# Kernel tuning notes

Hardware: AMD Instinct MI355X
Metric: run time of the kernel (lower is better)

Reference implementation:

```python
import jax, jax.numpy as jnp
import numpy as np

K = 16  # neighbors

def _pdist2(a, b):
    # squared euclidean distances (B,N,M); same argsort order as torch.cdist
    return (jnp.sum(a * a, -1)[:, :, None] + jnp.sum(b * b, -1)[:, None, :]
            - 2.0 * jnp.einsum('bnd,bmd->bnm', a, b))

def _knn(xyz, k):
    d2 = jax.lax.stop_gradient(_pdist2(xyz, xyz))
    return jax.lax.top_k(-d2, k)[1]  # (B,N,k) smallest distances

_gather_f = jax.vmap(lambda f, i: f[:, i])  # feat (C,N), idx (...,) -> (C,...)
_gather_x = jax.vmap(lambda x, i: x[i])     # xyz (N,D), idx (...,) -> (...,D)

def _bn_act(x, g, b):
    # eval-mode BatchNorm (running_mean=0, running_var=1) folded to affine, + LeakyReLU(0.1)
    shp = (1, -1) + (1,) * (x.ndim - 2)
    return jax.nn.leaky_relu(x * g.reshape(shp) + b.reshape(shp), 0.1)

def _lfa(xyz, feat, idx, Wm, gm, bm, Ws, Wp, gp, bp):
    # xyz (B,N,3), feat (B,C,N), idx (B,N,K)
    neigh_feat = _gather_f(feat, idx)          # (B,C,N,K)
    neigh_xyz = _gather_x(xyz, idx)            # (B,N,K,3)
    center = xyz[:, :, None, :]
    diff = center - neigh_xyz
    dist = jnp.linalg.norm(diff, axis=-1, keepdims=True)
    rel = jnp.concatenate([diff, dist, jnp.broadcast_to(center, neigh_xyz.shape), neigh_xyz], axis=-1)
    rel = jnp.transpose(rel, (0, 3, 1, 2))     # (B,10,N,K)
    x = jnp.concatenate([neigh_feat, rel], axis=1)          # (B,C+10,N,K)
    x = _bn_act(jnp.einsum('oc,bcnk->bonk', Wm, x), gm, bm)  # (B,O,N,K)
    a = jax.nn.softmax(jnp.einsum('oc,bcnk->bonk', Ws, x), axis=3)
    x = jnp.sum(x * a, axis=3)                               # attentive pool over K -> (B,O,N)
    return _bn_act(jnp.einsum('oc,bcn->bon', Wp, x), gp, bp)

def _interp(src_xyz, src_feat, tgt_xyz):
    nn_idx = jnp.argmin(jax.lax.stop_gradient(_pdist2(tgt_xyz, src_xyz)), axis=-1)  # (B,N)
    return _gather_f(src_feat, nn_idx)  # (B,C,N)


def setup_inputs() -> dict:
    key = jax.random.key(0)
    ks = jax.random.split(key, 24)
    B, N, CIN, NC = 2, 8192, 6, 13
    M1, M2 = N // 2, N // 4
    w = lambda i, shp: jax.random.normal(ks[i], shp, jnp.float32) * 0.05
    ones = lambda c: jnp.ones((c,), jnp.float32)
    zeros = lambda c: jnp.zeros((c,), jnp.float32)
    inp = {
        'xyz': jax.random.uniform(ks[0], (B, N, 3), jnp.float32),
        'feat': jax.random.normal(ks[1], (B, N, CIN), jnp.float32),
        'sel1': jax.random.randint(ks[2], (B, M1), 0, N),
        'sel2': jax.random.randint(ks[3], (B, M2), 0, M1),
        'Wpre': w(4, (64, CIN)), 'gpre': ones(64), 'bpre': zeros(64),
        'W1m': w(5, (64, 74)), 'g1m': ones(64), 'b1m': zeros(64),
        'W1s': w(6, (64, 64)), 'W1p': w(7, (64, 64)), 'g1p': ones(64), 'b1p': zeros(64),
        'W2m': w(8, (128, 74)), 'g2m': ones(128), 'b2m': zeros(128),
        'W2s': w(9, (128, 128)), 'W2p': w(10, (128, 128)), 'g2p': ones(128), 'b2p': zeros(128),
        'W3m': w(11, (256, 138)), 'g3m': ones(256), 'b3m': zeros(256),
        'W3s': w(12, (256, 256)), 'W3p': w(13, (256, 256)), 'g3p': ones(256), 'b3p': zeros(256),
        'Wu2': w(14, (128, 384)), 'gu2': ones(128), 'bu2': zeros(128),
        'Wu1': w(15, (64, 192)), 'gu1': ones(64), 'bu1': zeros(64),
        'Wh1': w(16, (64, 64)), 'bh1': zeros(64),
        'Wh2': w(17, (NC, 64)), 'bh2': zeros(NC),
    }
    return inp


def reference(xyz, feat, sel1, sel2, Wpre, gpre, bpre,
              W1m, g1m, b1m, W1s, W1p, g1p, b1p,
              W2m, g2m, b2m, W2s, W2p, g2p, b2p,
              W3m, g3m, b3m, W3s, W3p, g3p, b3p,
              Wu2, gu2, bu2, Wu1, gu1, bu1,
              Wh1, bh1, Wh2, bh2):
    ft = jnp.transpose(feat, (0, 2, 1))                       # (B,Cin,N)
    x0 = _bn_act(jnp.einsum('oc,bcn->bon', Wpre, ft), gpre, bpre)
    n0 = _knn(xyz, K)
    x1 = _lfa(xyz, x0, n0, W1m, g1m, b1m, W1s, W1p, g1p, b1p)  # (B,64,N)
    xyz1 = _gather_x(xyz, sel1); f1 = _gather_f(x1, sel1)      # random downsample 0.5
    n1 = _knn(xyz1, K)
    x2 = _lfa(xyz1, f1, n1, W2m, g2m, b2m, W2s, W2p, g2p, b2p)  # (B,128,M1)
    xyz2 = _gather_x(xyz1, sel2); f2 = _gather_f(x2, sel2)
    n2 = _knn(xyz2, K)
    x3 = _lfa(xyz2, f2, n2, W3m, g3m, b3m, W3s, W3p, g3p, b3p)  # (B,256,M2)
    up2 = _interp(xyz2, x3, xyz1)
    d2 = _bn_act(jnp.einsum('oc,bcn->bon', Wu2, jnp.concatenate([up2, x2], 1)), gu2, bu2)
    up1 = _interp(xyz1, d2, xyz)
    d1 = _bn_act(jnp.einsum('oc,bcn->bon', Wu1, jnp.concatenate([up1, x1], 1)), gu1, bu1)
    h = jax.nn.leaky_relu(jnp.einsum('oc,bcn->bon', Wh1, d1) + bh1[None, :, None], 0.1)
    logits = jnp.einsum('oc,bcn->bon', Wh2, h) + bh2[None, :, None]
    return jnp.transpose(logits, (0, 2, 1))                    # (B,N,num_classes)
```

## Files before the change

kernel.cpp:

```cpp
#include <hip/hip_runtime.h>
#include <hip/hip_bf16.h>

#pragma clang fp contract(off)

typedef unsigned long long ull;

__device__ __forceinline__ float lrelu(float v) { return v >= 0.0f ? v : 0.1f * v; }

__device__ __forceinline__ float sumsq3(float x, float y, float z) {
    return ((x * x) + (y * y)) + (z * z);
}

__device__ __forceinline__ float dot3fma(float ax, float ay, float az,
                                         float bx, float by, float bz) {
    float d = ax * bx;
    d = __builtin_fmaf(ay, by, d);
    d = __builtin_fmaf(az, bz, d);
    return d;
}

__device__ __forceinline__ float distf(float qn, float sn, float dot) {
    float s = qn + sn;
    return __builtin_fmaf(-2.0f, dot, s);
}

__device__ __forceinline__ ull packkey(float d, int i) {
    unsigned u = __float_as_uint(d);
    u = (u & 0x80000000u) ? ~u : (u | 0x80000000u);
    return ((ull)u << 32) | (unsigned)i;
}

__device__ __forceinline__ ull shfl_xor_u64(ull v, int mask) {
    int lo = __shfl_xor((int)(v & 0xffffffffull), mask);
    int hi = __shfl_xor((int)(v >> 32), mask);
    return ((ull)(unsigned)hi << 32) | (unsigned)lo;
}

__device__ __forceinline__ void cswap64(ull& x, ull& y) {
    bool sw = y < x;
    ull lo = sw ? y : x;
    ull hi = sw ? x : y;
    x = lo; y = hi;
}

__device__ __forceinline__ ull min64(ull a, ull b) { return a < b ? a : b; }

__global__ void k_pre(const float* __restrict__ feat, const float* __restrict__ W,
                      const float* __restrict__ g, const float* __restrict__ bb,
                      float* __restrict__ x0) {
    int p = blockIdx.x * blockDim.x + threadIdx.x;
    if (p >= 2 * 8192) return;
    const float* f = feat + (size_t)p * 6;
    float fv[6];
#pragma unroll
    for (int c = 0; c < 6; ++c) fv[c] = f[c];
    float* out = x0 + (size_t)p * 64;
    for (int o = 0; o < 64; ++o) {
        float s = 0.0f;
#pragma unroll
        for (int c = 0; c < 6; ++c) s = __builtin_fmaf(W[o * 6 + c], fv[c], s);
        float v = s * g[o];
        v = v + bb[o];
        out[o] = lrelu(v);
    }
}

__global__ void k_wt(const float* __restrict__ W, float* __restrict__ WT, int M, int K) {
    int i = blockIdx.x * 256 + threadIdx.x;
    if (i >= M * K) return;
    int o = i / K, c = i - o * K;
    WT[c * M + o] = W[i];
}

template <int LPQ, int TS>
__launch_bounds__(256)
__global__ void k_knn_reg(const float* __restrict__ xyz, int* __restrict__ out_idx, int Npts) {
    constexpr int QPB = 256 / LPQ;
    __shared__ float4 sp[TS];
    int b = blockIdx.y;
    int tid = threadIdx.x;
    int qi = tid / LPQ;
    int l = tid % LPQ;
    int q = blockIdx.x * QPB + qi;
    const float* X = xyz + (size_t)b * Npts * 3;
    float qx = X[q * 3], qy = X[q * 3 + 1], qz = X[q * 3 + 2];
    float qn = sumsq3(qx, qy, qz);

    ull key[16];
#pragma unroll
    for (int u = 0; u < 16; ++u) key[u] = ~0ull;
    ull p0 = ~0ull, p1 = ~0ull, p2 = ~0ull, p3 = ~0ull;
    int cnt = 0;
    float tau_d = INFINITY;

    auto merge = [&]() {
        cswap64(p0, p2); cswap64(p1, p3); cswap64(p0, p1);
        cswap64(p2, p3); cswap64(p1, p2);
        key[12] = min64(key[12], p3);
        key[13] = min64(key[13], p2);
        key[14] = min64(key[14], p1);
        key[15] = min64(key[15], p0);
#pragma unroll
        for (int dstep = 8; dstep >= 1; dstep >>= 1) {
#pragma unroll
            for (int i = 0; i < 16; ++i) {
                if (!(i & dstep)) cswap64(key[i], key[i + dstep]);
            }
        }
        p0 = p1 = p2 = p3 = ~0ull;
        cnt = 0;
        ull t = key[15];
#pragma unroll
        for (int mask = 1; mask < LPQ; mask <<= 1) t = min64(t, shfl_xor_u64(t, mask));
        unsigned hu = (unsigned)(t >> 32);
        unsigned fb = (hu & 0x80000000u) ? (hu & 0x7fffffffu) : ~hu;
        tau_d = (hu == 0xffffffffu) ? INFINITY : __uint_as_float(fb);
    };

    for (int t0 = 0; t0 < Npts; t0 += TS) {
        __syncthreads();
        for (int j = tid; j < TS; j += 256) {
            int i = t0 + j;
            float px = X[i * 3], py = X[i * 3 + 1], pz = X[i * 3 + 2];
            sp[j] = make_float4(px, py, pz, sumsq3(px, py, pz));
        }
        __syncthreads();
        for (int j = l; j < TS; j += LPQ) {
            float4 p = sp[j];
            float d = distf(qn, p.w, dot3fma(qx, qy, qz, p.x, p.y, p.z));
            if (d <= tau_d) {
                p3 = p2; p2 = p1; p1 = p0;
                p0 = packkey(d, t0 + j);
                ++cnt;
            }
            if (__any(cnt >= 4)) merge();
        }
    }
    if (__any(cnt > 0)) merge();

    for (int mask = 1; mask < LPQ; mask <<= 1) {
        ull ok[16];
#pragma unroll
        for (int i = 0; i < 16; ++i) ok[i] = shfl_xor_u64(key[15 - i], mask);
#pragma unroll
        for (int i = 0; i < 16; ++i) key[i] = min64(ok[i], key[i]);
#pragma unroll
        for (int dstep = 8; dstep >= 1; dstep >>= 1) {
#pragma unroll
            for (int i = 0; i < 16; ++i) {
                if (!(i & dstep)) cswap64(key[i], key[i + dstep]);
            }
        }
    }

    if (l == 0) {
        int* o = out_idx + ((size_t)b * Npts + q) * 16;
#pragma unroll
        for (int u = 0; u < 16; ++u) o[u] = (int)(unsigned)(key[u] & 0xffffffffull);
    }
}

template <int C>
__global__ void k_gather(const float* __restrict__ src_xyz, const float* __restrict__ src_feat,
                         const int* __restrict__ sel, float* __restrict__ dst_xyz,
                         float* __restrict__ dst_feat, int M, int Nsrc) {
    int b = blockIdx.y, m = blockIdx.x;
    int s = sel[(size_t)b * M + m];
    const float* fx = src_xyz + ((size_t)b * Nsrc + s) * 3;
    const float* ff = src_feat + ((size_t)b * Nsrc + s) * C;
    float* dx = dst_xyz + ((size_t)b * M + m) * 3;
    float* df = dst_feat + ((size_t)b * M + m) * C;
    if (threadIdx.x < 3) dx[threadIdx.x] = fx[threadIdx.x];
    for (int c = threadIdx.x; c < C; c += blockDim.x) df[c] = ff[c];
}

template <int CIN, int COUT, int NCOL>
__launch_bounds__(256)
__global__ void k_lfa(const float* __restrict__ xyz, const float* __restrict__ feat,
                      const int* __restrict__ kn,
                      const float* __restrict__ WmT, const float* __restrict__ gm, const float* __restrict__ bm,
                      const float* __restrict__ WsT,
                      const float* __restrict__ WpT, const float* __restrict__ gp, const float* __restrict__ bp,
                      float* __restrict__ outf, int Npts) {
    constexpr int CR = CIN + 10;
    constexpr int PPB = NCOL / 16;
    constexpr int RT = COUT / 16;
    constexpr int CT = NCOL / 16;
    constexpr int TPG = 16 / CT;
    constexpr int BUFR = (CR > COUT) ? CR : COUT;
    __shared__ float buf[BUFR * NCOL];
    int b = blockIdx.y, tid = threadIdx.x;
    int n0 = blockIdx.x * PPB;
    const float* X = xyz + (size_t)b * Npts * 3;

    {
        constexpr int TPC = 256 / NCOL;
        int jl = tid % NCOL;
        int cp = tid / NCOL;
        int n = n0 + (jl >> 4);
        int k = jl & 15;
        int nbr = kn[((size_t)b * Npts + n) * 16 + k];
        const float* fr = feat + ((size_t)b * Npts + nbr) * CIN;
        for (int c = cp; c < CIN; c += TPC) buf[c * NCOL + jl] = fr[c];
        if (cp == 0) {
            float cx = X[n * 3], cy = X[n * 3 + 1], cz = X[n * 3 + 2];
            float nx = X[nbr * 3], ny = X[nbr * 3 + 1], nz = X[nbr * 3 + 2];
            float dx = cx - nx, dy = cy - ny, dz = cz - nz;
            float dn = sqrtf(sumsq3(dx, dy, dz));
            buf[(CIN + 0) * NCOL + jl] = dx; buf[(CIN + 1) * NCOL + jl] = dy;
            buf[(CIN + 2) * NCOL + jl] = dz; buf[(CIN + 3) * NCOL + jl] = dn;
            buf[(CIN + 4) * NCOL + jl] = cx; buf[(CIN + 5) * NCOL + jl] = cy;
            buf[(CIN + 6) * NCOL + jl] = cz; buf[(CIN + 7) * NCOL + jl] = nx;
            buf[(CIN + 8) * NCOL + jl] = ny; buf[(CIN + 9) * NCOL + jl] = nz;
        }
    }
    __syncthreads();

    int tx = tid & 15, ty = tid >> 4;
    float acc[RT][CT];
#pragma unroll
    for (int r = 0; r < RT; ++r)
#pragma unroll
        for (int cc = 0; cc < CT; ++cc) acc[r][cc] = 0.0f;

    for (int c = 0; c < CR; ++c) {
        float a[RT], bv[CT];
#pragma unroll
        for (int r4 = 0; r4 < RT; r4 += 4)
            *reinterpret_cast<float4*>(&a[r4]) =
                *reinterpret_cast<const float4*>(&WmT[c * COUT + ty * RT + r4]);
#pragma unroll
        for (int c4 = 0; c4 < CT; c4 += 4)
            *reinterpret_cast<float4*>(&bv[c4]) =
                *reinterpret_cast<const float4*>(&buf[c * NCOL + tx * CT + c4]);
#pragma unroll
        for (int r = 0; r < RT; ++r)
#pragma unroll
            for (int cc = 0; cc < CT; ++cc)
                acc[r][cc] = __builtin_fmaf(a[r], bv[cc], acc[r][cc]);
    }
    __syncthreads();
#pragma unroll
    for (int r = 0; r < RT; ++r) {
        int o = ty * RT + r;
        float gg = gm[o], bbv = bm[o];
#pragma unroll
        for (int cc = 0; cc < CT; ++cc) {
            float v = acc[r][cc] * gg;
            v = v + bbv;
            buf[o * NCOL + tx * CT + cc] = lrelu(v);
        }
    }
    __syncthreads();

#pragma unroll
    for (int r = 0; r < RT; ++r)
#pragma unroll
        for (int cc = 0; cc < CT; ++cc) acc[r][cc] = 0.0f;
    for (int c = 0; c < COUT; ++c) {
        float a[RT], bv[CT];
#pragma unroll
        for (int r4 = 0; r4 < RT; r4 += 4)
            *reinterpret_cast<float4*>(&a[r4]) =
                *reinterpret_cast<const float4*>(&WsT[c * COUT + ty * RT + r4]);
#pragma unroll
        for (int c4 = 0; c4 < CT; c4 += 4)
            *reinterpret_cast<float4*>(&bv[c4]) =
                *reinterpret_cast<const float4*>(&buf[c * NCOL + tx * CT + c4]);
#pragma unroll
        for (int r = 0; r < RT; ++r)
#pragma unroll
            for (int cc = 0; cc < CT; ++cc)
                acc[r][cc] = __builtin_fmaf(a[r], bv[cc], acc[r][cc]);
    }
    float pwv[RT];
#pragma unroll
    for (int r = 0; r < RT; ++r) {
        int o = ty * RT + r;
        float m = acc[r][0];
#pragma unroll
        for (int cc = 1; cc < CT; ++cc) m = fmaxf(m, acc[r][cc]);
#pragma unroll
        for (int mask = 1; mask < TPG; mask <<= 1) m = fmaxf(m, __shfl_xor(m, mask));
        float e[CT]; float ps = 0.0f;
#pragma unroll
        for (int cc = 0; cc < CT; ++cc) { e[cc] = expf(acc[r][cc] - m); ps = ps + e[cc]; }
        float tot = ps;
#pragma unroll
        for (int mask = 1; mask < TPG; mask <<= 1) tot = tot + __shfl_xor(tot, mask);
        float pw = 0.0f;
#pragma unroll
        for (int cc = 0; cc < CT; ++cc) {
            float a_ = e[cc] / tot;
            float t = buf[o * NCOL + tx * CT + cc] * a_;
            pw = pw + t;
        }
#pragma unroll
        for (int mask = 1; mask < TPG; mask <<= 1) pw = pw + __shfl_xor(pw, mask);
        pwv[r] = pw;
    }
    __syncthreads();
    if (tx % TPG == 0) {
        int pt = tx / TPG;
#pragma unroll
        for (int r = 0; r < RT; ++r) buf[(ty * RT + r) * PPB + pt] = pwv[r];
    }
    __syncthreads();

    constexpr int NOUT = (COUT * PPB) / 256;
    constexpr int PSTEP = 256 / COUT;
    int o = tid % COUT;
    int pbase = tid / COUT;
    float sacc[NOUT];
#pragma unroll
    for (int u = 0; u < NOUT; ++u) sacc[u] = 0.0f;
    for (int c = 0; c < COUT; ++c) {
        float wv = WpT[c * COUT + o];
#pragma unroll
        for (int u = 0; u < NOUT; ++u)
            sacc[u] = __builtin_fmaf(wv, buf[c * PPB + pbase + u * PSTEP], sacc[u]);
    }
    float gg = gp[o], bbv = bp[o];
#pragma unroll
    for (int u = 0; u < NOUT; ++u) {
        float v = sacc[u] * gg;
        v = v + bbv;
        int p = pbase + u * PSTEP;
        outf[((size_t)b * Npts + n0 + p) * COUT + o] = lrelu(v);
    }
}

template <int LPQ, int TS>
__launch_bounds__(256)
__global__ void k_nn_par(const float* __restrict__ tgt, const float* __restrict__ src,
                         int* __restrict__ nn, int Mt, int Ms) {
    constexpr int QPB = 256 / LPQ;
    __shared__ float4 sp[TS];
    int b = blockIdx.y;
    int tid = threadIdx.x;
    int qi = tid / LPQ;
    int l = tid % LPQ;
    int q = blockIdx.x * QPB + qi;
    const float* T = tgt + (size_t)b * Mt * 3;
    const float* S = src + (size_t)b * Ms * 3;
    float qx = T[q * 3], qy = T[q * 3 + 1], qz = T[q * 3 + 2];
    float qn = sumsq3(qx, qy, qz);
    float bd = INFINITY; int bi = 0x7fffffff;
    for (int t0 = 0; t0 < Ms; t0 += TS) {
        __syncthreads();
        for (int j = tid; j < TS; j += 256) {
            int i = t0 + j;
            float px = S[i * 3], py = S[i * 3 + 1], pz = S[i * 3 + 2];
            sp[j] = make_float4(px, py, pz, sumsq3(px, py, pz));
        }
        __syncthreads();
        for (int j = l; j < TS; j += LPQ) {
            float4 p = sp[j];
            float d = distf(qn, p.w, dot3fma(qx, qy, qz, p.x, p.y, p.z));
            if (d < bd) { bd = d; bi = t0 + j; }
        }
    }
#pragma unroll
    for (int s = LPQ / 2; s; s >>= 1) {
        float od = __shfl_xor(bd, s);
        int oi = __shfl_xor(bi, s);
        bool better = (od < bd) || ((od == bd) && (oi < bi));
        bd = better ? od : bd;
        bi = better ? oi : bi;
    }
    if (l == 0) nn[(size_t)b * Mt + q] = bi;
}

template <int CSRC, int CSKIP, int COUT>
__global__ void k_up(const float* __restrict__ srcf, const float* __restrict__ skipf,
                     const int* __restrict__ nn,
                     const float* __restrict__ W, const float* __restrict__ g, const float* __restrict__ bb,
                     float* __restrict__ outf, int Mt, int Ms) {
    __shared__ float fin[CSRC + CSKIP];
    int b = blockIdx.y, n = blockIdx.x, tid = threadIdx.x;
    int j = nn[(size_t)b * Mt + n];
    const float* fs = srcf + ((size_t)b * Ms + j) * CSRC;
    const float* fk = skipf + ((size_t)b * Mt + n) * CSKIP;
    for (int c = tid; c < CSRC; c += blockDim.x) fin[c] = fs[c];
    for (int c = tid; c < CSKIP; c += blockDim.x) fin[CSRC + c] = fk[c];
    __syncthreads();
    for (int o = tid; o < COUT; o += blockDim.x) {
        const float* wr = W + (size_t)o * (CSRC + CSKIP);
        float s = 0.0f;
        for (int c = 0; c < CSRC + CSKIP; ++c) s = __builtin_fmaf(wr[c], fin[c], s);
        float v = s * g[o]; v = v + bb[o];
        outf[((size_t)b * Mt + n) * COUT + o] = lrelu(v);
    }
}

__global__ void k_u1head(const float* __restrict__ srcf, const float* __restrict__ skipf,
                         const int* __restrict__ nn,
                         const float* __restrict__ Wu1, const float* __restrict__ gu1, const float* __restrict__ bu1,
                         const float* __restrict__ Wh1, const float* __restrict__ bh1,
                         const float* __restrict__ Wh2, const float* __restrict__ bh2,
                         float* __restrict__ out, int Mt, int Ms) {
    __shared__ float fin[192];
    __shared__ float d1[64];
    __shared__ float h[64];
    int b = blockIdx.y, n = blockIdx.x, tid = threadIdx.x;
    int j = nn[(size_t)b * Mt + n];
    const float* fs = srcf + ((size_t)b * Ms + j) * 128;
    const float* fk = skipf + ((size_t)b * Mt + n) * 64;
    for (int c = tid; c < 128; c += 64) fin[c] = fs[c];
    fin[128 + tid] = fk[tid];
    __syncthreads();
    {
        const float* wr = Wu1 + (size_t)tid * 192;
        float s = 0.0f;
        for (int c = 0; c < 192; ++c) s = __builtin_fmaf(wr[c], fin[c], s);
        float v = s * gu1[tid]; v = v + bu1[tid];
        d1[tid] = lrelu(v);
    }
    __syncthreads();
    {
        const float* wr = Wh1 + (size_t)tid * 64;
        float s = 0.0f;
        for (int c = 0; c < 64; ++c) s = __builtin_fmaf(wr[c], d1[c], s);
        float v = s + bh1[tid];
        h[tid] = lrelu(v);
    }
    __syncthreads();
    if (tid < 13) {
        const float* wr = Wh2 + (size_t)tid * 64;
        float s = 0.0f;
        for (int c = 0; c < 64; ++c) s = __builtin_fmaf(wr[c], h[c], s);
        out[((size_t)b * Mt + n) * 13 + tid] = s + bh2[tid];
    }
}

extern "C" void kernel_launch(void* const* d_in, const int* in_sizes, int n_in,
                              void* d_out, int out_size, void* d_ws, size_t ws_size,
                              hipStream_t stream) {
    const float* xyz  = (const float*)d_in[0];
    const float* feat = (const float*)d_in[1];
    const int*   sel1 = (const int*)d_in[2];
    const int*   sel2 = (const int*)d_in[3];
    const float* Wpre = (const float*)d_in[4];
    const float* gpre = (const float*)d_in[5];
    const float* bpre = (const float*)d_in[6];
    const float* W1m  = (const float*)d_in[7];
    const float* g1m  = (const float*)d_in[8];
    const float* b1m  = (const float*)d_in[9];
    const float* W1s  = (const float*)d_in[10];
    const float* W1p  = (const float*)d_in[11];
    const float* g1p  = (const float*)d_in[12];
    const float* b1p  = (const float*)d_in[13];
    const float* W2m  = (const float*)d_in[14];
    const float* g2m  = (const float*)d_in[15];
    const float* b2m  = (const float*)d_in[16];
    const float* W2s  = (const float*)d_in[17];
    const float* W2p  = (const float*)d_in[18];
    const float* g2p  = (const float*)d_in[19];
    const float* b2p  = (const float*)d_in[20];
    const float* W3m  = (const float*)d_in[21];
    const float* g3m  = (const float*)d_in[22];
    const float* b3m  = (const float*)d_in[23];
    const float* W3s  = (const float*)d_in[24];
    const float* W3p  = (const float*)d_in[25];
    const float* g3p  = (const float*)d_in[26];
    const float* b3p  = (const float*)d_in[27];
    const float* Wu2  = (const float*)d_in[28];
    const float* gu2  = (const float*)d_in[29];
    const float* bu2  = (const float*)d_in[30];
    const float* Wu1  = (const float*)d_in[31];
    const float* gu1  = (const float*)d_in[32];
    const float* bu1  = (const float*)d_in[33];
    const float* Wh1  = (const float*)d_in[34];
    const float* bh1  = (const float*)d_in[35];
    const float* Wh2  = (const float*)d_in[36];
    const float* bh2  = (const float*)d_in[37];
    float* out = (float*)d_out;

    char* w = (char*)d_ws;
    auto alloc = [&](size_t n) { char* p = w; w += (n + 255) & ~(size_t)255; return p; };
    float* x0   = (float*)alloc((size_t)2 * 8192 * 64 * 4);
    float* x1   = (float*)alloc((size_t)2 * 8192 * 64 * 4);
    float* f1   = (float*)alloc((size_t)2 * 4096 * 64 * 4);
    float* x2   = (float*)alloc((size_t)2 * 4096 * 128 * 4);
    float* f2   = (float*)alloc((size_t)2 * 2048 * 128 * 4);
    float* x3   = (float*)alloc((size_t)2 * 2048 * 256 * 4);
    float* d2f  = (float*)alloc((size_t)2 * 4096 * 128 * 4);
    float* xyz1 = (float*)alloc((size_t)2 * 4096 * 3 * 4);
    float* xyz2 = (float*)alloc((size_t)2 * 2048 * 3 * 4);
    int* n0   = (int*)alloc((size_t)2 * 8192 * 16 * 4);
    int* n1   = (int*)alloc((size_t)2 * 4096 * 16 * 4);
    int* n2   = (int*)alloc((size_t)2 * 2048 * 16 * 4);
    int* nnu2 = (int*)alloc((size_t)2 * 4096 * 4);
    int* nnu1 = (int*)alloc((size_t)2 * 8192 * 4);
    float* WmT1 = (float*)alloc((size_t)74 * 64 * 4);
    float* WsT1 = (float*)alloc((size_t)64 * 64 * 4);
    float* WpT1 = (float*)alloc((size_t)64 * 64 * 4);
    float* WmT2 = (float*)alloc((size_t)74 * 128 * 4);
    float* WsT2 = (float*)alloc((size_t)128 * 128 * 4);
    float* WpT2 = (float*)alloc((size_t)128 * 128 * 4);
    float* WmT3 = (float*)alloc((size_t)138 * 256 * 4);
    float* WsT3 = (float*)alloc((size_t)256 * 256 * 4);
    float* WpT3 = (float*)alloc((size_t)256 * 256 * 4);

    k_pre<<<128, 128, 0, stream>>>(feat, Wpre, gpre, bpre, x0);
    k_wt<<<(64 * 74 + 255) / 256, 256, 0, stream>>>(W1m, WmT1, 64, 74);
    k_wt<<<(64 * 64 + 255) / 256, 256, 0, stream>>>(W1s, WsT1, 64, 64);
    k_wt<<<(64 * 64 + 255) / 256, 256, 0, stream>>>(W1p, WpT1, 64, 64);
    k_wt<<<(128 * 74 + 255) / 256, 256, 0, stream>>>(W2m, WmT2, 128, 74);
    k_wt<<<(128 * 128 + 255) / 256, 256, 0, stream>>>(W2s, WsT2, 128, 128);
    k_wt<<<(128 * 128 + 255) / 256, 256, 0, stream>>>(W2p, WpT2, 128, 128);
    k_wt<<<(256 * 138 + 255) / 256, 256, 0, stream>>>(W3m, WmT3, 256, 138);
    k_wt<<<(256 * 256 + 255) / 256, 256, 0, stream>>>(W3s, WsT3, 256, 256);
    k_wt<<<(256 * 256 + 255) / 256, 256, 0, stream>>>(W3p, WpT3, 256, 256);

    k_knn_reg<32, 1024><<<dim3(1024, 2), 256, 0, stream>>>(xyz, n0, 8192);
    k_lfa<64, 64, 128><<<dim3(8192 / 8, 2), 256, 0, stream>>>(
        xyz, x0, n0, WmT1, g1m, b1m, WsT1, WpT1, g1p, b1p, x1, 8192);

    k_gather<64><<<dim3(4096, 2), 64, 0, stream>>>(xyz, x1, sel1, xyz1, f1, 4096, 8192);
    k_knn_reg<32, 1024><<<dim3(512, 2), 256, 0, stream>>>(xyz1, n1, 4096);
    k_lfa<64, 128, 128><<<dim3(4096 / 8, 2), 256, 0, stream>>>(
        xyz1, f1, n1, WmT2, g2m, b2m, WsT2, WpT2, g2p, b2p, x2, 4096);

    k_gather<128><<<dim3(2048, 2), 64, 0, stream>>>(xyz1, x2, sel2, xyz2, f2, 2048, 4096);
    k_knn_reg<32, 1024><<<dim3(256, 2), 256, 0, stream>>>(xyz2, n2, 2048);
    k_lfa<128, 256, 64><<<dim3(2048 / 4, 2), 256, 0, stream>>>(
        xyz2, f2, n2, WmT3, g3m, b3m, WsT3, WpT3, g3p, b3p, x3, 2048);

    k_nn_par<16, 512><<<dim3(256, 2), 256, 0, stream>>>(xyz1, xyz2, nnu2, 4096, 2048);
    k_up<256, 128, 128><<<dim3(4096, 2), 128, 0, stream>>>(x3, x2, nnu2, Wu2, gu2, bu2,
                                                           d2f, 4096, 2048);
    k_nn_par<16, 512><<<dim3(512, 2), 256, 0, stream>>>(xyz, xyz1, nnu1, 8192, 4096);
    k_u1head<<<dim3(8192, 2), 64, 0, stream>>>(d2f, x1, nnu1, Wu1, gu1, bu1, Wh1, bh1,
                                               Wh2, bh2, out, 8192, 4096);
}
```

Measured before the change: 1.180 ms.

## Restructure LFA kernel to one column per lane with wave-uniform weight rows

```diff
diff --git a/kernel.cpp b/kernel.cpp
--- a/kernel.cpp
+++ b/kernel.cpp
@@ -174,34 +174,33 @@
     for (int c = threadIdx.x; c < C; c += blockDim.x) df[c] = ff[c];
 }
 
-template <int CIN, int COUT, int NCOL>
-__launch_bounds__(256)
+template <int CIN, int COUT>
+__launch_bounds__(512)
 __global__ void k_lfa(const float* __restrict__ xyz, const float* __restrict__ feat,
                       const int* __restrict__ kn,
                       const float* __restrict__ WmT, const float* __restrict__ gm, const float* __restrict__ bm,
                       const float* __restrict__ WsT,
                       const float* __restrict__ WpT, const float* __restrict__ gp, const float* __restrict__ bp,
                       float* __restrict__ outf, int Npts) {
+    constexpr int NCOL = 64;
     constexpr int CR = CIN + 10;
     constexpr int PPB = NCOL / 16;
-    constexpr int RT = COUT / 16;
-    constexpr int CT = NCOL / 16;
-    constexpr int TPG = 16 / CT;
+    constexpr int RT = COUT / 8;
     constexpr int BUFR = (CR > COUT) ? CR : COUT;
-    __shared__ float buf[BUFR * NCOL];
+    static_assert(RT % 4 == 0, "geom");
+    __shared__ __align__(16) float buf[BUFR * NCOL];
     int b = blockIdx.y, tid = threadIdx.x;
     int n0 = blockIdx.x * PPB;
     const float* X = xyz + (size_t)b * Npts * 3;
 
     {
-        constexpr int TPC = 256 / NCOL;
-        int jl = tid % NCOL;
-        int cp = tid / NCOL;
+        int jl = tid & 63;
+        int cp = tid >> 6;
         int n = n0 + (jl >> 4);
         int k = jl & 15;
         int nbr = kn[((size_t)b * Npts + n) * 16 + k];
         const float* fr = feat + ((size_t)b * Npts + nbr) * CIN;
-        for (int c = cp; c < CIN; c += TPC) buf[c * NCOL + jl] = fr[c];
+        for (int c = cp; c < CIN; c += 8) buf[c * NCOL + jl] = fr[c];
         if (cp == 0) {
             float cx = X[n * 3], cy = X[n * 3 + 1], cz = X[n * 3 + 2];
             float nx = X[nbr * 3], ny = X[nbr * 3 + 1], nz = X[nbr * 3 + 2];
@@ -216,99 +215,85 @@
     }
     __syncthreads();
 
-    int tx = tid & 15, ty = tid >> 4;
-    float acc[RT][CT];
-#pragma unroll
-    for (int r = 0; r < RT; ++r)
-#pragma unroll
-        for (int cc = 0; cc < CT; ++cc) acc[r][cc] = 0.0f;
-
+    int tx = tid & 63;
+    int ty = __builtin_amdgcn_readfirstlane(tid >> 6);
+
+    float acc[RT];
+#pragma unroll
+    for (int r = 0; r < RT; ++r) acc[r] = 0.0f;
+
+#pragma unroll 2
     for (int c = 0; c < CR; ++c) {
-        float a[RT], bv[CT];
+        float bv = buf[c * NCOL + tx];
+        const float* wr = WmT + c * COUT + ty * RT;
+        float a[RT];
 #pragma unroll
         for (int r4 = 0; r4 < RT; r4 += 4)
             *reinterpret_cast<float4*>(&a[r4]) =
-                *reinterpret_cast<const float4*>(&WmT[c * COUT + ty * RT + r4]);
-#pragma unroll
-        for (int c4 = 0; c4 < CT; c4 += 4)
-            *reinterpret_cast<float4*>(&bv[c4]) =
-                *reinterpret_cast<const float4*>(&buf[c * NCOL + tx * CT + c4]);
+                *reinterpret_cast<const float4*>(&wr[r4]);
 #pragma unroll
         for (int r = 0; r < RT; ++r)
-#pragma unroll
-            for (int cc = 0; cc < CT; ++cc)
-                acc[r][cc] = __builtin_fmaf(a[r], bv[cc], acc[r][cc]);
+            acc[r] = __builtin_fmaf(a[r], bv, acc[r]);
     }
     __syncthreads();
 #pragma unroll
     for (int r = 0; r < RT; ++r) {
         int o = ty * RT + r;
-        float gg = gm[o], bbv = bm[o];
-#pragma unroll
-        for (int cc = 0; cc < CT; ++cc) {
-            float v = acc[r][cc] * gg;
-            v = v + bbv;
-            buf[o * NCOL + tx * CT + cc] = lrelu(v);
-        }
-    }
-    __syncthreads();
-
-#pragma unroll
-    for (int r = 0; r < RT; ++r)
-#pragma unroll
-        for (int cc = 0; cc < CT; ++cc) acc[r][cc] = 0.0f;
+        float v = acc[r] * gm[o];
+        v = v + bm[o];
+        buf[o * NCOL + tx] = lrelu(v);
+    }
+    __syncthreads();
+
+    float s2[RT];
+#pragma unroll
+    for (int r = 0; r < RT; ++r) s2[r] = 0.0f;
+#pragma unroll 2
     for (int c = 0; c < COUT; ++c) {
-        float a[RT], bv[CT];
+        float bv = buf[c * NCOL + tx];
+        const float* wr = WsT + c * COUT + ty * RT;
+        float a[RT];
 #pragma unroll
         for (int r4 = 0; r4 < RT; r4 += 4)
             *reinterpret_cast<float4*>(&a[r4]) =
-                *reinterpret_cast<const float4*>(&WsT[c * COUT + ty * RT + r4]);
-#pragma unroll
-        for (int c4 = 0; c4 < CT; c4 += 4)
-            *reinterpret_cast<float4*>(&bv[c4]) =
-                *reinterpret_cast<const float4*>(&buf[c * NCOL + tx * CT + c4]);
+                *reinterpret_cast<const float4*>(&wr[r4]);
 #pragma unroll
         for (int r = 0; r < RT; ++r)
-#pragma unroll
-            for (int cc = 0; cc < CT; ++cc)
-                acc[r][cc] = __builtin_fmaf(a[r], bv[cc], acc[r][cc]);
+            s2[r] = __builtin_fmaf(a[r], bv, s2[r]);
     }
     float pwv[RT];
 #pragma unroll
     for (int r = 0; r < RT; ++r) {
         int o = ty * RT + r;
-        float m = acc[r][0];
-#pragma unroll
-        for (int cc = 1; cc < CT; ++cc) m = fmaxf(m, acc[r][cc]);
-#pragma unroll
-        for (int mask = 1; mask < TPG; mask <<= 1) m = fmaxf(m, __shfl_xor(m, mask));
-        float e[CT]; float ps = 0.0f;
-#pragma unroll
-        for (int cc = 0; cc < CT; ++cc) { e[cc] = expf(acc[r][cc] - m); ps = ps + e[cc]; }
-        float tot = ps;
-#pragma unroll
-        for (int mask = 1; mask < TPG; mask <<= 1) tot = tot + __shfl_xor(tot, mask);
-        float pw = 0.0f;
-#pragma unroll
-        for (int cc = 0; cc < CT; ++cc) {
-            float a_ = e[cc] / tot;
-            float t = buf[o * NCOL + tx * CT + cc] * a_;
-            pw = pw + t;
-        }
-#pragma unroll
-        for (int mask = 1; mask < TPG; mask <<= 1) pw = pw + __shfl_xor(pw, mask);
+        float m = s2[r];
+        m = fmaxf(m, __shfl_xor(m, 1));
+        m = fmaxf(m, __shfl_xor(m, 2));
+        m = fmaxf(m, __shfl_xor(m, 4));
+        m = fmaxf(m, __shfl_xor(m, 8));
+        float e = expf(s2[r] - m);
+        float tot = e;
+        tot = tot + __shfl_xor(tot, 1);
+        tot = tot + __shfl_xor(tot, 2);
+        tot = tot + __shfl_xor(tot, 4);
+        tot = tot + __shfl_xor(tot, 8);
+        float a_ = e / tot;
+        float pw = buf[o * NCOL + tx] * a_;
+        pw = pw + __shfl_xor(pw, 1);
+        pw = pw + __shfl_xor(pw, 2);
+        pw = pw + __shfl_xor(pw, 4);
+        pw = pw + __shfl_xor(pw, 8);
         pwv[r] = pw;
     }
     __syncthreads();
-    if (tx % TPG == 0) {
-        int pt = tx / TPG;
+    if ((tx & 15) == 0) {
+        int pt = tx >> 4;
 #pragma unroll
         for (int r = 0; r < RT; ++r) buf[(ty * RT + r) * PPB + pt] = pwv[r];
     }
     __syncthreads();
 
-    constexpr int NOUT = (COUT * PPB) / 256;
-    constexpr int PSTEP = 256 / COUT;
+    constexpr int TPP = 512 / COUT;
+    constexpr int NOUT = (PPB + TPP - 1) / TPP;
     int o = tid % COUT;
     int pbase = tid / COUT;
     float sacc[NOUT];
@@ -317,16 +302,20 @@
     for (int c = 0; c < COUT; ++c) {
         float wv = WpT[c * COUT + o];
 #pragma unroll
-        for (int u = 0; u < NOUT; ++u)
-            sacc[u] = __builtin_fmaf(wv, buf[c * PPB + pbase + u * PSTEP], sacc[u]);
+        for (int u = 0; u < NOUT; ++u) {
+            int p = pbase + u * TPP;
+            if (p < PPB) sacc[u] = __builtin_fmaf(wv, buf[c * PPB + p], sacc[u]);
+        }
     }
     float gg = gp[o], bbv = bp[o];
 #pragma unroll
     for (int u = 0; u < NOUT; ++u) {
-        float v = sacc[u] * gg;
-        v = v + bbv;
-        int p = pbase + u * PSTEP;
-        outf[((size_t)b * Npts + n0 + p) * COUT + o] = lrelu(v);
+        int p = pbase + u * TPP;
+        if (p < PPB) {
+            float v = sacc[u] * gg;
+            v = v + bbv;
+            outf[((size_t)b * Npts + n0 + p) * COUT + o] = lrelu(v);
+        }
     }
 }
 
@@ -514,17 +503,17 @@
     k_wt<<<(256 * 256 + 255) / 256, 256, 0, stream>>>(W3p, WpT3, 256, 256);
 
     k_knn_reg<32, 1024><<<dim3(1024, 2), 256, 0, stream>>>(xyz, n0, 8192);
-    k_lfa<64, 64, 128><<<dim3(8192 / 8, 2), 256, 0, stream>>>(
+    k_lfa<64, 64><<<dim3(8192 / 4, 2), 512, 0, stream>>>(
         xyz, x0, n0, WmT1, g1m, b1m, WsT1, WpT1, g1p, b1p, x1, 8192);
 
     k_gather<64><<<dim3(4096, 2), 64, 0, stream>>>(xyz, x1, sel1, xyz1, f1, 4096, 8192);
     k_knn_reg<32, 1024><<<dim3(512, 2), 256, 0, stream>>>(xyz1, n1, 4096);
-    k_lfa<64, 128, 128><<<dim3(4096 / 8, 2), 256, 0, stream>>>(
+    k_lfa<64, 128><<<dim3(4096 / 4, 2), 512, 0, stream>>>(
         xyz1, f1, n1, WmT2, g2m, b2m, WsT2, WpT2, g2p, b2p, x2, 4096);
 
     k_gather<128><<<dim3(2048, 2), 64, 0, stream>>>(xyz1, x2, sel2, xyz2, f2, 2048, 4096);
     k_knn_reg<32, 1024><<<dim3(256, 2), 256, 0, stream>>>(xyz2, n2, 2048);
-    k_lfa<128, 256, 64><<<dim3(2048 / 4, 2), 256, 0, stream>>>(
+    k_lfa<128, 256><<<dim3(2048 / 4, 2), 512, 0, stream>>>(
         xyz2, f2, n2, WmT3, g3m, b3m, WsT3, WpT3, g3p, b3p, x3, 2048);
 
     k_nn_par<16, 512><<<dim3(256, 2), 256, 0, stream>>>(xyz1, xyz2, nnu2, 4096, 2048);
```

After: 1.237 ms. +4.9%, slower.
